# Optimization experiments

Measured on AMD Instinct MI355X. Metric: run time of the kernel, lower is better.

Reference implementation:

```python
import jax, jax.numpy as jnp
import numpy as np

SEARCH = (4, 6, 8)

def _round_ste(v):
    return v + jax.lax.stop_gradient(jnp.round(v) - v)

def _fake_quant(x, alpha, k_bits):
    # PAMS quant_act: clamp to [-alpha, alpha], uniform fake-quant with STE round
    a = jnp.abs(alpha)
    s = (2.0 ** (k_bits - 1) - 1.0) / a
    return _round_ste(jnp.clip(x, -a, a) * s) / s

def setup_inputs() -> dict:
    key = jax.random.key(0)
    k0, k1 = jax.random.split(key, 2)
    B, C, H, W = 16, 64, 256, 256
    x = jax.random.normal(k0, (B, C, H, W), jnp.float32)
    grad_feat = jax.random.normal(k1, (B, 2), jnp.float32)
    bits = jnp.zeros((B,), jnp.float32)
    weighted_bits = jnp.zeros((B,), jnp.float32)
    Wl = jnp.ones((3, C + 2), jnp.float32)              # nn.init.ones_
    bl = jnp.array([0.0, 0.0, 1.0], jnp.float32)        # zeros_, bias[-1]=1
    alpha1 = jnp.full((1,), 10.0, jnp.float32)          # PAMS alpha init
    alpha2 = jnp.full((1,), 10.0, jnp.float32)
    alpha3 = jnp.full((1,), 10.0, jnp.float32)
    return dict(x=x, grad_feat=grad_feat, bits=bits, weighted_bits=weighted_bits,
                Wl=Wl, bl=bl, alpha1=alpha1, alpha2=alpha2, alpha3=alpha3)

def reference(x, grad_feat, bits, weighted_bits, Wl, bl, alpha1, alpha2, alpha3):
    sg = jax.lax.stop_gradient
    # std over spatial dims, unbiased (torch default), detached -> [B, C]
    layer_std = sg(jnp.std(x, axis=(2, 3), ddof=1))
    x_embed = jnp.concatenate([grad_feat, layer_std], axis=1)   # [B, C+2]
    bit_type = x_embed @ Wl.T + bl                              # [B, 3]
    flag = jnp.argmax(bit_type, axis=1)                         # [B]
    p = jax.nn.softmax(bit_type, axis=1)
    p1, p2, p3 = p[:, 0], p[:, 1], p[:, 2]
    bits_hard = ((flag == 0) * SEARCH[0] + (flag == 1) * SEARCH[1]
                 + (flag == 2) * SEARCH[2]).astype(x.dtype)
    bits_soft = p1 * SEARCH[0] + p2 * SEARCH[1] + p3 * SEARCH[2]
    bits_out = sg(bits_hard) - sg(bits_soft) + bits_soft        # STE on bit count
    bits = bits + bits_out
    denom = sg(SEARCH[0] * p1 + SEARCH[1] * p2 + SEARCH[2] * p3)
    weighted_bits = weighted_bits + bits_out / denom
    q1 = _fake_quant(x, alpha1[0], SEARCH[0])
    q2 = _fake_quant(x, alpha2[0], SEARCH[1])
    q3 = _fake_quant(x, alpha3[0], SEARCH[2])
    w1 = p1[:, None, None, None]; w2 = p2[:, None, None, None]; w3 = p3[:, None, None, None]
    out_soft = w1 * q1 + w2 * q2 + w3 * q3
    m1 = (flag == 0)[:, None, None, None].astype(x.dtype)
    m2 = (flag == 1)[:, None, None, None].astype(x.dtype)
    m3 = (flag == 2)[:, None, None, None].astype(x.dtype)
    out_hard = m1 * q1 + m2 * q2 + m3 * q3
    residual = sg(out_hard) - sg(out_soft) + out_soft           # STE hard/soft gate
    return grad_feat, residual, bits, weighted_bits
```

## Files before the change

kernel.cpp:

```cpp
#include <hip/hip_runtime.h>
#include <math.h>

typedef float fx4 __attribute__((ext_vector_type(4)));
#define TPB  256
#define NBLK 1024

__global__ __launch_bounds__(TPB)
void bitsel_rq_kernel(const fx4* __restrict__ x,
                      const float* __restrict__ gf,
                      const float* __restrict__ bits_in,
                      const float* __restrict__ wbits_in,
                      const float* __restrict__ Wl,
                      const float* __restrict__ bl,
                      const float* __restrict__ a1,
                      const float* __restrict__ a2,
                      const float* __restrict__ a3,
                      float* __restrict__ out,
                      fx4* __restrict__ res,
                      float* __restrict__ part,
                      int gR, int gQ, int mode,
                      int B, int C, int n4, size_t Ntot) {
    const int j   = blockIdx.x;
    const int tid = threadIdx.x;
    const int GB  = B / 2;
    const int GBC = GB * C;
    const int sl4 = (GBC * n4) / NBLK;
    const int spc = n4 / sl4;
    const int bpb = NBLK / GB;

    int isR, slice;
    if (mode == 0)      { isR = 1;     slice = j;      }
    else if (mode == 2) { isR = 0;     slice = j;      }
    else                { isR = j & 1; slice = j >> 1; }

    if (isR) {
        const int ch  = slice / spc;
        const int sub = slice % spc;
        const size_t base = (size_t)(gR * GBC + ch) * (size_t)n4 + (size_t)sub * sl4;
        float sum = 0.f, sq = 0.f;
        #pragma unroll 4
        for (int i = tid; i < sl4; i += TPB) {
            fx4 v = x[base + i];
            sum += (v.x + v.y) + (v.z + v.w);
            sq  += v.x * v.x + v.y * v.y + v.z * v.z + v.w * v.w;
        }
        for (int off = 32; off > 0; off >>= 1) {
            sum += __shfl_down(sum, off);
            sq  += __shfl_down(sq,  off);
        }
        __shared__ float ssum[4], ssq[4];
        if ((tid & 63) == 0) { ssum[tid >> 6] = sum; ssq[tid >> 6] = sq; }
        __syncthreads();
        if (tid == 0) {
            float S  = ssum[0] + ssum[1] + ssum[2] + ssum[3];
            float Qq = ssq[0]  + ssq[1]  + ssq[2]  + ssq[3];
            const size_t pidx = ((size_t)(gR * GBC + ch) * spc + sub) * 2;
            part[pidx + 0] = S;
            part[pidx + 1] = Qq;
        }
    } else {
        const int bl_ = slice / bpb;
        const int b   = gQ * GB + bl_;

        __shared__ float s_std[64];
        __shared__ float s_as[2];

        if (tid < C) {
            const size_t pbase = ((size_t)(gQ * GBC + bl_ * C + tid)) * spc * 2;
            float S = 0.f, Qq = 0.f;
            #pragma unroll
            for (int p = 0; p < spc; ++p) {
                S  += part[pbase + 2 * p + 0];
                Qq += part[pbase + 2 * p + 1];
            }
            const float N = (float)n4 * 4.f;
            float var = (Qq - S * S / N) / (N - 1.f);
            s_std[tid] = sqrtf(fmaxf(var, 0.f));
        }
        __syncthreads();
        if (tid == 0) {
            const int D = C + 2;
            float bt[3];
            for (int kk = 0; kk < 3; ++kk) {
                float acc = gf[2 * b] * Wl[kk * D] + gf[2 * b + 1] * Wl[kk * D + 1];
                for (int cc = 0; cc < C; ++cc) acc += s_std[cc] * Wl[kk * D + 2 + cc];
                bt[kk] = acc + bl[kk];
            }
            int flag = 0; float m = bt[0];
            if (bt[1] > m) { m = bt[1]; flag = 1; }
            if (bt[2] > m) { m = bt[2]; flag = 2; }
            float e0 = expf(bt[0] - m), e1 = expf(bt[1] - m), e2 = expf(bt[2] - m);
            float esum = e0 + e1 + e2;
            float p1 = e0 / esum, p2 = e1 / esum, p3 = e2 / esum;
            float bits_hard = (flag == 0) ? 4.f : (flag == 1) ? 6.f : 8.f;
            float bits_soft = 4.f * p1 + 6.f * p2 + 8.f * p3;
            float bits_out  = (bits_hard - bits_soft) + bits_soft;
            float denom     = 4.f * p1 + 6.f * p2 + 8.f * p3;
            float alpha = (flag == 0) ? a1[0] : (flag == 1) ? a2[0] : a3[0];
            float a  = fabsf(alpha);
            float sc = (exp2f(bits_hard - 1.f) - 1.f) / a;
            s_as[0] = a; s_as[1] = sc;
            if ((slice % bpb) == 0) {
                out[2 * b]     = gf[2 * b];
                out[2 * b + 1] = gf[2 * b + 1];
                out[2 * B + Ntot + b]     = bits_in[b] + bits_out;
                out[2 * B + Ntot + B + b] = wbits_in[b] + bits_out / denom;
            }
        }
        __syncthreads();
        const float a  = s_as[0];
        const float sc = s_as[1];
        const size_t base = (size_t)gQ * GBC * (size_t)n4 + (size_t)slice * sl4;
        #pragma unroll 4
        for (int i = tid; i < sl4; i += TPB) {
            fx4 v = x[base + i];
            fx4 r;
            r.x = rintf(fminf(fmaxf(v.x, -a), a) * sc) / sc;
            r.y = rintf(fminf(fmaxf(v.y, -a), a) * sc) / sc;
            r.z = rintf(fminf(fmaxf(v.z, -a), a) * sc) / sc;
            r.w = rintf(fminf(fmaxf(v.w, -a), a) * sc) / sc;
            __builtin_nontemporal_store(r, &res[base + i]);
        }
    }
}

extern "C" void kernel_launch(void* const* d_in, const int* in_sizes, int n_in,
                              void* d_out, int out_size, void* d_ws, size_t ws_size,
                              hipStream_t stream) {
    const float* x     = (const float*)d_in[0];
    const float* gf    = (const float*)d_in[1];
    const float* bits  = (const float*)d_in[2];
    const float* wbits = (const float*)d_in[3];
    const float* Wl    = (const float*)d_in[4];
    const float* bl    = (const float*)d_in[5];
    const float* a1    = (const float*)d_in[6];
    const float* a2    = (const float*)d_in[7];
    const float* a3    = (const float*)d_in[8];
    float* out = (float*)d_out;

    const int B   = in_sizes[2];
    const int C   = in_sizes[4] / 3 - 2;
    const int HWn = in_sizes[0] / (B * C);
    const int n4  = HWn / 4;
    const size_t Ntot = (size_t)in_sizes[0];

    float* part = (float*)d_ws;
    fx4*   res  = (fx4*)(out + 2 * B);

    bitsel_rq_kernel<<<NBLK, TPB, 0, stream>>>(
        (const fx4*)x, gf, bits, wbits, Wl, bl, a1, a2, a3,
        out, res, part, 0, -1, 0, B, C, n4, Ntot);
    bitsel_rq_kernel<<<2 * NBLK, TPB, 0, stream>>>(
        (const fx4*)x, gf, bits, wbits, Wl, bl, a1, a2, a3,
        out, res, part, 1, 0, 1, B, C, n4, Ntot);
    bitsel_rq_kernel<<<NBLK, TPB, 0, stream>>>(
        (const fx4*)x, gf, bits, wbits, Wl, bl, a1, a2, a3,
        out, res, part, -1, 1, 2, B, C, n4, Ntot);
}
```

Measured before the change: 142.7 us.

## Pipeline reduce and quantize across four launches with uneven batch groups

Replaces the two-half-batch, three-launch schedule with four launches over batch groups of 4, 6 and 6. Each middle launch quantizes the previous group while reducing the next, so the first and last launches that do only one phase are smaller. Slice size and slices per channel are now compile-time constants (4096 fx4 and 4), which hardcodes the assumption HW=65536. The quantize pass also switches to nontemporal loads of x. The trade-off is one extra launch boundary and loss of generality to other shapes.

```diff
diff --git a/kernel.cpp b/kernel.cpp
--- a/kernel.cpp
+++ b/kernel.cpp
@@ -2,8 +2,9 @@
 #include <math.h>
 
 typedef float fx4 __attribute__((ext_vector_type(4)));
-#define TPB  256
-#define NBLK 1024
+#define TPB 256
+#define SL4 4096
+#define SPC 4
 
 __global__ __launch_bounds__(TPB)
 void bitsel_rq_kernel(const fx4* __restrict__ x,
@@ -18,28 +19,21 @@
                       float* __restrict__ out,
                       fx4* __restrict__ res,
                       float* __restrict__ part,
-                      int gR, int gQ, int mode,
+                      int bR0, int bQ0, int nQblk,
                       int B, int C, int n4, size_t Ntot) {
-    const int j   = blockIdx.x;
     const int tid = threadIdx.x;
-    const int GB  = B / 2;
-    const int GBC = GB * C;
-    const int sl4 = (GBC * n4) / NBLK;
-    const int spc = n4 / sl4;
-    const int bpb = NBLK / GB;
+    const int spb = C * SPC;
 
-    int isR, slice;
-    if (mode == 0)      { isR = 1;     slice = j;      }
-    else if (mode == 2) { isR = 0;     slice = j;      }
-    else                { isR = j & 1; slice = j >> 1; }
-
-    if (isR) {
-        const int ch  = slice / spc;
-        const int sub = slice % spc;
-        const size_t base = (size_t)(gR * GBC + ch) * (size_t)n4 + (size_t)sub * sl4;
+    if ((int)blockIdx.x >= nQblk) {
+        const int slice = (int)blockIdx.x - nQblk;
+        const int b   = bR0 + slice / spb;
+        const int sib = slice % spb;
+        const int ch  = sib / SPC;
+        const int sub = sib % SPC;
+        const size_t base = (size_t)(b * C + ch) * (size_t)n4 + (size_t)sub * SL4;
         float sum = 0.f, sq = 0.f;
         #pragma unroll 4
-        for (int i = tid; i < sl4; i += TPB) {
+        for (int i = tid; i < SL4; i += TPB) {
             fx4 v = x[base + i];
             sum += (v.x + v.y) + (v.z + v.w);
             sq  += v.x * v.x + v.y * v.y + v.z * v.z + v.w * v.w;
@@ -54,22 +48,23 @@
         if (tid == 0) {
             float S  = ssum[0] + ssum[1] + ssum[2] + ssum[3];
             float Qq = ssq[0]  + ssq[1]  + ssq[2]  + ssq[3];
-            const size_t pidx = ((size_t)(gR * GBC + ch) * spc + sub) * 2;
+            const size_t pidx = ((size_t)(b * C + ch) * SPC + sub) * 2;
             part[pidx + 0] = S;
             part[pidx + 1] = Qq;
         }
     } else {
-        const int bl_ = slice / bpb;
-        const int b   = gQ * GB + bl_;
+        const int slice = (int)blockIdx.x;
+        const int b   = bQ0 + slice / spb;
+        const int sib = slice % spb;
 
         __shared__ float s_std[64];
         __shared__ float s_as[2];
 
         if (tid < C) {
-            const size_t pbase = ((size_t)(gQ * GBC + bl_ * C + tid)) * spc * 2;
+            const size_t pbase = ((size_t)(b * C + tid)) * SPC * 2;
             float S = 0.f, Qq = 0.f;
             #pragma unroll
-            for (int p = 0; p < spc; ++p) {
+            for (int p = 0; p < SPC; ++p) {
                 S  += part[pbase + 2 * p + 0];
                 Qq += part[pbase + 2 * p + 1];
             }
@@ -100,7 +95,7 @@
             float a  = fabsf(alpha);
             float sc = (exp2f(bits_hard - 1.f) - 1.f) / a;
             s_as[0] = a; s_as[1] = sc;
-            if ((slice % bpb) == 0) {
+            if (sib == 0) {
                 out[2 * b]     = gf[2 * b];
                 out[2 * b + 1] = gf[2 * b + 1];
                 out[2 * B + Ntot + b]     = bits_in[b] + bits_out;
@@ -110,10 +105,12 @@
         __syncthreads();
         const float a  = s_as[0];
         const float sc = s_as[1];
-        const size_t base = (size_t)gQ * GBC * (size_t)n4 + (size_t)slice * sl4;
+        const int ch  = sib / SPC;
+        const int sub = sib % SPC;
+        const size_t base = (size_t)(b * C + ch) * (size_t)n4 + (size_t)sub * SL4;
         #pragma unroll 4
-        for (int i = tid; i < sl4; i += TPB) {
-            fx4 v = x[base + i];
+        for (int i = tid; i < SL4; i += TPB) {
+            fx4 v = __builtin_nontemporal_load(&x[base + i]);
             fx4 r;
             r.x = rintf(fminf(fmaxf(v.x, -a), a) * sc) / sc;
             r.y = rintf(fminf(fmaxf(v.y, -a), a) * sc) / sc;
@@ -143,17 +140,23 @@
     const int HWn = in_sizes[0] / (B * C);
     const int n4  = HWn / 4;
     const size_t Ntot = (size_t)in_sizes[0];
+    const int spb = C * SPC;
 
     float* part = (float*)d_ws;
     fx4*   res  = (fx4*)(out + 2 * B);
 
-    bitsel_rq_kernel<<<NBLK, TPB, 0, stream>>>(
+    const int g0 = 4, g1 = 6, g2 = 6;
+
+    bitsel_rq_kernel<<<g0 * spb, TPB, 0, stream>>>(
         (const fx4*)x, gf, bits, wbits, Wl, bl, a1, a2, a3,
-        out, res, part, 0, -1, 0, B, C, n4, Ntot);
-    bitsel_rq_kernel<<<2 * NBLK, TPB, 0, stream>>>(
+        out, res, part, 0, 0, 0, B, C, n4, Ntot);
+    bitsel_rq_kernel<<<g0 * spb + g1 * spb, TPB, 0, stream>>>(
         (const fx4*)x, gf, bits, wbits, Wl, bl, a1, a2, a3,
-        out, res, part, 1, 0, 1, B, C, n4, Ntot);
-    bitsel_rq_kernel<<<NBLK, TPB, 0, stream>>>(
+        out, res, part, g0, 0, g0 * spb, B, C, n4, Ntot);
+    bitsel_rq_kernel<<<g1 * spb + g2 * spb, TPB, 0, stream>>>(
         (const fx4*)x, gf, bits, wbits, Wl, bl, a1, a2, a3,
-        out, res, part, -1, 1, 2, B, C, n4, Ntot);
+        out, res, part, g0 + g1, g0, g1 * spb, B, C, n4, Ntot);
+    bitsel_rq_kernel<<<g2 * spb, TPB, 0, stream>>>(
+        (const fx4*)x, gf, bits, wbits, Wl, bl, a1, a2, a3,
+        out, res, part, 0, g0 + g1, g2 * spb, B, C, n4, Ntot);
 }
```

New measurement: 138.1 us. 3.2% less time.
